# Performance work log

Hardware: AMD Instinct MI355X
Metric: run time of the kernel (lower is better)

## Reference

```python
import jax, jax.numpy as jnp
import numpy as np

THRESHOLD = 1e-12
B = 2_000_000


def _q_to_matrix(q):
    # q: [B,4] = (qw,qx,qy,qz) -> [B,3,3]
    qw, qx, qy, qz = q[:, 0], q[:, 1], q[:, 2], q[:, 3]
    r00 = 1 - 2 * (qy * qy + qz * qz)
    r01 = 2 * (qx * qy - qz * qw)
    r02 = 2 * (qx * qz + qy * qw)
    r10 = 2 * (qx * qy + qz * qw)
    r11 = 1 - 2 * (qx * qx + qz * qz)
    r12 = 2 * (qy * qz - qx * qw)
    r20 = 2 * (qx * qz - qy * qw)
    r21 = 2 * (qy * qz + qx * qw)
    r22 = 1 - 2 * (qx * qx + qy * qy)
    return jnp.stack([
        jnp.stack([r00, r01, r02], axis=-1),
        jnp.stack([r10, r11, r12], axis=-1),
        jnp.stack([r20, r21, r22], axis=-1),
    ], axis=-2)


def _so3_RV(omega):
    # omega: [B,3] -> (R [B,3,3], V [B,3,3]) via Rodrigues
    ox, oy, oz = omega[:, 0], omega[:, 1], omega[:, 2]
    z = jnp.zeros_like(ox)
    K = jnp.stack([
        jnp.stack([z, -oz, oy], axis=-1),
        jnp.stack([oz, z, -ox], axis=-1),
        jnp.stack([-oy, ox, z], axis=-1),
    ], axis=-2)
    K2 = jnp.matmul(K, K)
    theta_sqr = ox * ox + oy * oy + oz * oz
    safe = theta_sqr > THRESHOLD
    ts = jnp.where(safe, theta_sqr, 1.0)  # avoid div by ~0
    theta = jnp.sqrt(ts)
    st, ct = jnp.sin(theta), jnp.cos(theta)
    A = jnp.where(safe, st / theta, 1.0)              # sin(t)/t
    Bc = jnp.where(safe, (1.0 - ct) / ts, 0.0)        # (1-cos t)/t^2
    Cc = jnp.where(safe, (theta - st) / (ts * theta), 1.0 / 6.0)  # (t-sin t)/t^3
    I = jnp.eye(3, dtype=omega.dtype)
    R = I + A[:, None, None] * K + Bc[:, None, None] * K2
    V = I + Bc[:, None, None] * K + Cc[:, None, None] * K2
    return R, V


def _M_to_R7(M):
    # M: [B,4,4] -> [B,7,1] (x,y,z,qw,qx,qy,qz), branchless quaternion extraction
    m = lambda i, j: M[:, i, j]
    c_m22 = m(2, 2) < 0
    c_0g1 = m(0, 0) > m(1, 1)
    c_0ln1 = m(0, 0) < -m(1, 1)
    s1 = c_m22 & c_0g1
    s2 = c_m22 & (~c_0g1)
    s3 = (~c_m22) & c_0ln1
    t1 = 1 + m(0, 0) - m(1, 1) - m(2, 2)
    t2 = 1 - m(0, 0) + m(1, 1) - m(2, 2)
    t3 = 1 - m(0, 0) - m(1, 1) + m(2, 2)
    t4 = 1 + m(0, 0) + m(1, 1) + m(2, 2)
    q1 = jnp.stack([m(2, 1) - m(1, 2), t1, m(0, 1) + m(1, 0), m(2, 0) + m(0, 2)], axis=-1)
    q2 = jnp.stack([m(0, 2) - m(2, 0), m(0, 1) + m(1, 0), t2, m(1, 2) + m(2, 1)], axis=-1)
    q3 = jnp.stack([m(1, 0) - m(0, 1), m(2, 0) + m(0, 2), m(1, 2) + m(2, 1), t3], axis=-1)
    q4 = jnp.stack([t4, m(2, 1) - m(1, 2), m(0, 2) - m(2, 0), m(1, 0) - m(0, 1)], axis=-1)
    t = jnp.where(s1, t1, jnp.where(s2, t2, jnp.where(s3, t3, t4)))
    q = jnp.where(s1[:, None], q1, jnp.where(s2[:, None], q2, jnp.where(s3[:, None], q3, q4)))
    q = q * (0.5 / jnp.sqrt(t))[:, None]
    q = jnp.where((q[:, 0] < 0)[:, None], -q, q)
    r7 = jnp.concatenate([M[:, 0:3, 3], q], axis=-1)
    return r7[:, :, None]


def setup_inputs() -> dict:
    key = jax.random.key(0)
    k1, k2, k3 = jax.random.split(key, 3)
    trans = jax.random.normal(k1, (B, 3), dtype=jnp.float32)
    q = jax.random.normal(k2, (B, 4), dtype=jnp.float32)
    q = q / jnp.linalg.norm(q, axis=1, keepdims=True)  # valid unit quaternion
    Tg = jnp.concatenate([trans, q], axis=1)[:, :, None]  # [B,7,1]
    xi = (0.5 * jax.random.normal(k3, (B, 6), dtype=jnp.float32))[:, :, None]  # [B,6,1]
    return {"Tg": Tg, "xi": xi}


def reference(Tg, xi):
    rho = xi[:, 0:3]          # [B,3,1]
    omega = xi[:, 3:6, 0]     # [B,3]
    R, V = _so3_RV(omega)
    top = jnp.concatenate([R, jnp.matmul(V, rho)], axis=-1)  # [B,3,4]
    bottom = jnp.broadcast_to(jnp.array([[[0.0, 0.0, 0.0, 1.0]]], dtype=Tg.dtype), (Tg.shape[0], 1, 4))
    Txi = jnp.concatenate([top, bottom], axis=-2)            # [B,4,4]
    Rg = _q_to_matrix(Tg[:, 3:7, 0])
    tg = Tg[:, 0:3]
    Tg_top = jnp.concatenate([Rg, tg], axis=-1)
    Tg_M = jnp.concatenate([Tg_top, bottom], axis=-2)        # [B,4,4]
    T = jnp.matmul(Txi, Tg_M)
    return _M_to_R7(T)
```

## Files before the change

### kernel.cpp

```cpp
#include <hip/hip_runtime.h>
#include <math.h>

__global__ __launch_bounds__(256) void se3comp_kernel(
    const float* __restrict__ Tg, const float* __restrict__ xi,
    float* __restrict__ out, int n)
{
    int i = blockIdx.x * blockDim.x + threadIdx.x;
    if (i >= n) return;

    const float2* x2 = reinterpret_cast<const float2*>(xi) + (size_t)i * 3;
    float2 a0 = x2[0], a1 = x2[1], a2 = x2[2];
    float rx = a0.x, ry = a0.y, rz = a1.x;
    float ox = a1.y, oy = a2.x, oz = a2.y;

    float th2 = ox*ox + oy*oy + oz*oz;
    bool safe = th2 > 1e-12f;
    float ts = safe ? th2 : 1.0f;
    float theta = sqrtf(ts);
    float st = sinf(theta);
    float ct = cosf(theta);
    float A  = safe ? st / theta : 1.0f;
    float Bc = safe ? (1.0f - ct) / ts : 0.0f;
    float Cc = safe ? (theta - st) / (ts * theta) : (1.0f / 6.0f);

    float xx = ox*ox - th2, yy = oy*oy - th2, zz = oz*oz - th2;
    float xy = ox*oy, xz = ox*oz, yz = oy*oz;

    float r00 = 1.0f + Bc*xx;
    float r01 = Bc*xy - A*oz;
    float r02 = Bc*xz + A*oy;
    float r10 = Bc*xy + A*oz;
    float r11 = 1.0f + Bc*yy;
    float r12 = Bc*yz - A*ox;
    float r20 = Bc*xz - A*oy;
    float r21 = Bc*yz + A*ox;
    float r22 = 1.0f + Bc*zz;

    float v00 = 1.0f + Cc*xx;
    float v01 = Cc*xy - Bc*oz;
    float v02 = Cc*xz + Bc*oy;
    float v10 = Cc*xy + Bc*oz;
    float v11 = 1.0f + Cc*yy;
    float v12 = Cc*yz - Bc*ox;
    float v20 = Cc*xz - Bc*oy;
    float v21 = Cc*yz + Bc*ox;
    float v22 = 1.0f + Cc*zz;

    float txi0 = v00*rx + v01*ry + v02*rz;
    float txi1 = v10*rx + v11*ry + v12*rz;
    float txi2 = v20*rx + v21*ry + v22*rz;

    const float* g = Tg + (size_t)i * 7;
    float tg0 = g[0], tg1 = g[1], tg2 = g[2];
    float qw = g[3], qx = g[4], qy = g[5], qz = g[6];

    float g00 = 1.0f - 2.0f*(qy*qy + qz*qz);
    float g01 = 2.0f*(qx*qy - qz*qw);
    float g02 = 2.0f*(qx*qz + qy*qw);
    float g10 = 2.0f*(qx*qy + qz*qw);
    float g11 = 1.0f - 2.0f*(qx*qx + qz*qz);
    float g12 = 2.0f*(qy*qz - qx*qw);
    float g20 = 2.0f*(qx*qz - qy*qw);
    float g21 = 2.0f*(qy*qz + qx*qw);
    float g22 = 1.0f - 2.0f*(qx*qx + qy*qy);

    float m00 = r00*g00 + r01*g10 + r02*g20;
    float m01 = r00*g01 + r01*g11 + r02*g21;
    float m02 = r00*g02 + r01*g12 + r02*g22;
    float m10 = r10*g00 + r11*g10 + r12*g20;
    float m11 = r10*g01 + r11*g11 + r12*g21;
    float m12 = r10*g02 + r11*g12 + r12*g22;
    float m20 = r20*g00 + r21*g10 + r22*g20;
    float m21 = r20*g01 + r21*g11 + r22*g21;
    float m22 = r20*g02 + r21*g12 + r22*g22;

    float t0 = r00*tg0 + r01*tg1 + r02*tg2 + txi0;
    float t1 = r10*tg0 + r11*tg1 + r12*tg2 + txi1;
    float t2 = r20*tg0 + r21*tg1 + r22*tg2 + txi2;

    bool c_m22  = m22 < 0.0f;
    bool c_0g1  = m00 > m11;
    bool c_0ln1 = m00 < -m11;
    float t, qa, qb, qc, qd;
    if (c_m22) {
        if (c_0g1) {
            t = 1.0f + m00 - m11 - m22;
            qa = m21 - m12; qb = t;         qc = m01 + m10; qd = m20 + m02;
        } else {
            t = 1.0f - m00 + m11 - m22;
            qa = m02 - m20; qb = m01 + m10; qc = t;         qd = m12 + m21;
        }
    } else {
        if (c_0ln1) {
            t = 1.0f - m00 - m11 + m22;
            qa = m10 - m01; qb = m20 + m02; qc = m12 + m21; qd = t;
        } else {
            t = 1.0f + m00 + m11 + m22;
            qa = t;         qb = m21 - m12; qc = m02 - m20; qd = m10 - m01;
        }
    }
    float s = 0.5f / sqrtf(t);
    qa *= s; qb *= s; qc *= s; qd *= s;
    if (qa < 0.0f) { qa = -qa; qb = -qb; qc = -qc; qd = -qd; }

    float* o = out + (size_t)i * 7;
    o[0] = t0; o[1] = t1; o[2] = t2;
    o[3] = qa; o[4] = qb; o[5] = qc; o[6] = qd;
}

extern "C" void kernel_launch(void* const* d_in, const int* in_sizes, int n_in,
                              void* d_out, int out_size, void* d_ws, size_t ws_size,
                              hipStream_t stream) {
    const float* Tg = (const float*)d_in[0];
    const float* xi = (const float*)d_in[1];
    float* out = (float*)d_out;
    int n = in_sizes[0] / 7;
    const int block = 256;
    int grid = (n + block - 1) / block;
    hipLaunchKernelGGL(se3comp_kernel, dim3(grid), dim3(block), 0, stream,
                       Tg, xi, out, n);
}
```

Measured before the change: 29.61 us.

## Stage AoS inputs and outputs through LDS with coalesced float4 transfers

Each block now loads its contiguous slab of Tg and xi into shared memory with float4 global loads, computes per-element from LDS, writes results to an LDS buffer, then stores the block's output with coalesced float4 writes. The target is the uncoalesced stride-7 scalar loads and stores of the AoS layout. It adds two barriers, LDS bank conflicts on stride-7/6 accesses, and extra LDS usage that may reduce occupancy. The tail is handled by truncating to whole float4s, so with n divisible by 4 it is fine, but other n would drop trailing floats.

```diff
diff --git a/kernel.cpp b/kernel.cpp
--- a/kernel.cpp
+++ b/kernel.cpp
@@ -1,122 +1,164 @@
 #include <hip/hip_runtime.h>
 #include <math.h>
 
+#define BLOCK 256
+#define EPB   256
+
 __global__ __launch_bounds__(256) void se3comp_kernel(
-    const float* __restrict__ Tg, const float* __restrict__ xi,
-    float* __restrict__ out, int n)
+    const float4* __restrict__ Tg4, const float4* __restrict__ xi4,
+    float4* __restrict__ out4, int n)
 {
-    int i = blockIdx.x * blockDim.x + threadIdx.x;
-    if (i >= n) return;
+    __shared__ float sTg[EPB * 7];
+    __shared__ float sXi[EPB * 6];
+    __shared__ float sOut[EPB * 7];
 
-    const float2* x2 = reinterpret_cast<const float2*>(xi) + (size_t)i * 3;
-    float2 a0 = x2[0], a1 = x2[1], a2 = x2[2];
-    float rx = a0.x, ry = a0.y, rz = a1.x;
-    float ox = a1.y, oy = a2.x, oz = a2.y;
+    const int tid = threadIdx.x;
+    const int blockBase = blockIdx.x * EPB;
 
-    float th2 = ox*ox + oy*oy + oz*oz;
-    bool safe = th2 > 1e-12f;
-    float ts = safe ? th2 : 1.0f;
-    float theta = sqrtf(ts);
-    float st = sinf(theta);
-    float ct = cosf(theta);
-    float A  = safe ? st / theta : 1.0f;
-    float Bc = safe ? (1.0f - ct) / ts : 0.0f;
-    float Cc = safe ? (theta - st) / (ts * theta) : (1.0f / 6.0f);
-
-    float xx = ox*ox - th2, yy = oy*oy - th2, zz = oz*oz - th2;
-    float xy = ox*oy, xz = ox*oz, yz = oy*oz;
-
-    float r00 = 1.0f + Bc*xx;
-    float r01 = Bc*xy - A*oz;
-    float r02 = Bc*xz + A*oy;
-    float r10 = Bc*xy + A*oz;
-    float r11 = 1.0f + Bc*yy;
-    float r12 = Bc*yz - A*ox;
-    float r20 = Bc*xz - A*oy;
-    float r21 = Bc*yz + A*ox;
-    float r22 = 1.0f + Bc*zz;
-
-    float v00 = 1.0f + Cc*xx;
-    float v01 = Cc*xy - Bc*oz;
-    float v02 = Cc*xz + Bc*oy;
-    float v10 = Cc*xy + Bc*oz;
-    float v11 = 1.0f + Cc*yy;
-    float v12 = Cc*yz - Bc*ox;
-    float v20 = Cc*xz - Bc*oy;
-    float v21 = Cc*yz + Bc*ox;
-    float v22 = 1.0f + Cc*zz;
-
-    float txi0 = v00*rx + v01*ry + v02*rz;
-    float txi1 = v10*rx + v11*ry + v12*rz;
-    float txi2 = v20*rx + v21*ry + v22*rz;
-
-    const float* g = Tg + (size_t)i * 7;
-    float tg0 = g[0], tg1 = g[1], tg2 = g[2];
-    float qw = g[3], qx = g[4], qy = g[5], qz = g[6];
-
-    float g00 = 1.0f - 2.0f*(qy*qy + qz*qz);
-    float g01 = 2.0f*(qx*qy - qz*qw);
-    float g02 = 2.0f*(qx*qz + qy*qw);
-    float g10 = 2.0f*(qx*qy + qz*qw);
-    float g11 = 1.0f - 2.0f*(qx*qx + qz*qz);
-    float g12 = 2.0f*(qy*qz - qx*qw);
-    float g20 = 2.0f*(qx*qz - qy*qw);
-    float g21 = 2.0f*(qy*qz + qx*qw);
-    float g22 = 1.0f - 2.0f*(qx*qx + qy*qy);
-
-    float m00 = r00*g00 + r01*g10 + r02*g20;
-    float m01 = r00*g01 + r01*g11 + r02*g21;
-    float m02 = r00*g02 + r01*g12 + r02*g22;
-    float m10 = r10*g00 + r11*g10 + r12*g20;
-    float m11 = r10*g01 + r11*g11 + r12*g21;
-    float m12 = r10*g02 + r11*g12 + r12*g22;
-    float m20 = r20*g00 + r21*g10 + r22*g20;
-    float m21 = r20*g01 + r21*g11 + r22*g21;
-    float m22 = r20*g02 + r21*g12 + r22*g22;
-
-    float t0 = r00*tg0 + r01*tg1 + r02*tg2 + txi0;
-    float t1 = r10*tg0 + r11*tg1 + r12*tg2 + txi1;
-    float t2 = r20*tg0 + r21*tg1 + r22*tg2 + txi2;
-
-    bool c_m22  = m22 < 0.0f;
-    bool c_0g1  = m00 > m11;
-    bool c_0ln1 = m00 < -m11;
-    float t, qa, qb, qc, qd;
-    if (c_m22) {
-        if (c_0g1) {
-            t = 1.0f + m00 - m11 - m22;
-            qa = m21 - m12; qb = t;         qc = m01 + m10; qd = m20 + m02;
-        } else {
-            t = 1.0f - m00 + m11 - m22;
-            qa = m02 - m20; qb = m01 + m10; qc = t;         qd = m12 + m21;
-        }
-    } else {
-        if (c_0ln1) {
-            t = 1.0f - m00 - m11 + m22;
-            qa = m10 - m01; qb = m20 + m02; qc = m12 + m21; qd = t;
-        } else {
-            t = 1.0f + m00 + m11 + m22;
-            qa = t;         qb = m21 - m12; qc = m02 - m20; qd = m10 - m01;
+    const long tgF4Base  = (long)blockBase * 7 / 4;
+    const long tgF4Total = ((long)n * 7) / 4;
+    float4* sTg4 = reinterpret_cast<float4*>(sTg);
+    #pragma unroll
+    for (int k = 0; k < 2; ++k) {
+        int idx = tid + k * BLOCK;
+        if (idx < EPB * 7 / 4) {
+            long g = tgF4Base + idx;
+            if (g < tgF4Total) sTg4[idx] = Tg4[g];
         }
     }
-    float s = 0.5f / sqrtf(t);
-    qa *= s; qb *= s; qc *= s; qd *= s;
-    if (qa < 0.0f) { qa = -qa; qb = -qb; qc = -qc; qd = -qd; }
+    const long xiF4Base  = (long)blockBase * 6 / 4;
+    const long xiF4Total = ((long)n * 6) / 4;
+    float4* sXi4 = reinterpret_cast<float4*>(sXi);
+    #pragma unroll
+    for (int k = 0; k < 2; ++k) {
+        int idx = tid + k * BLOCK;
+        if (idx < EPB * 6 / 4) {
+            long g = xiF4Base + idx;
+            if (g < xiF4Total) sXi4[idx] = xi4[g];
+        }
+    }
+    __syncthreads();
 
-    float* o = out + (size_t)i * 7;
-    o[0] = t0; o[1] = t1; o[2] = t2;
-    o[3] = qa; o[4] = qb; o[5] = qc; o[6] = qd;
+    const int e = blockBase + tid;
+    if (e < n) {
+        const float* x = &sXi[tid * 6];
+        float rx = x[0], ry = x[1], rz = x[2];
+        float ox = x[3], oy = x[4], oz = x[5];
+        const float* gp = &sTg[tid * 7];
+        float tg0 = gp[0], tg1 = gp[1], tg2 = gp[2];
+        float qw = gp[3], qx = gp[4], qy = gp[5], qz = gp[6];
+
+        float th2 = ox*ox + oy*oy + oz*oz;
+        bool safe = th2 > 1e-12f;
+        float ts = safe ? th2 : 1.0f;
+        float theta = sqrtf(ts);
+        float st = sinf(theta);
+        float ct = cosf(theta);
+        float A  = safe ? st / theta : 1.0f;
+        float Bc = safe ? (1.0f - ct) / ts : 0.0f;
+        float Cc = safe ? (theta - st) / (ts * theta) : (1.0f / 6.0f);
+
+        float xx = ox*ox - th2, yy = oy*oy - th2, zz = oz*oz - th2;
+        float xy = ox*oy, xz = ox*oz, yz = oy*oz;
+
+        float r00 = 1.0f + Bc*xx;
+        float r01 = Bc*xy - A*oz;
+        float r02 = Bc*xz + A*oy;
+        float r10 = Bc*xy + A*oz;
+        float r11 = 1.0f + Bc*yy;
+        float r12 = Bc*yz - A*ox;
+        float r20 = Bc*xz - A*oy;
+        float r21 = Bc*yz + A*ox;
+        float r22 = 1.0f + Bc*zz;
+
+        float v00 = 1.0f + Cc*xx;
+        float v01 = Cc*xy - Bc*oz;
+        float v02 = Cc*xz + Bc*oy;
+        float v10 = Cc*xy + Bc*oz;
+        float v11 = 1.0f + Cc*yy;
+        float v12 = Cc*yz - Bc*ox;
+        float v20 = Cc*xz - Bc*oy;
+        float v21 = Cc*yz + Bc*ox;
+        float v22 = 1.0f + Cc*zz;
+
+        float txi0 = v00*rx + v01*ry + v02*rz;
+        float txi1 = v10*rx + v11*ry + v12*rz;
+        float txi2 = v20*rx + v21*ry + v22*rz;
+
+        float g00 = 1.0f - 2.0f*(qy*qy + qz*qz);
+        float g01 = 2.0f*(qx*qy - qz*qw);
+        float g02 = 2.0f*(qx*qz + qy*qw);
+        float g10 = 2.0f*(qx*qy + qz*qw);
+        float g11 = 1.0f - 2.0f*(qx*qx + qz*qz);
+        float g12 = 2.0f*(qy*qz - qx*qw);
+        float g20 = 2.0f*(qx*qz - qy*qw);
+        float g21 = 2.0f*(qy*qz + qx*qw);
+        float g22 = 1.0f - 2.0f*(qx*qx + qy*qy);
+
+        float m00 = r00*g00 + r01*g10 + r02*g20;
+        float m01 = r00*g01 + r01*g11 + r02*g21;
+        float m02 = r00*g02 + r01*g12 + r02*g22;
+        float m10 = r10*g00 + r11*g10 + r12*g20;
+        float m11 = r10*g01 + r11*g11 + r12*g21;
+        float m12 = r10*g02 + r11*g12 + r12*g22;
+        float m20 = r20*g00 + r21*g10 + r22*g20;
+        float m21 = r20*g01 + r21*g11 + r22*g21;
+        float m22 = r20*g02 + r21*g12 + r22*g22;
+
+        float t0 = r00*tg0 + r01*tg1 + r02*tg2 + txi0;
+        float t1 = r10*tg0 + r11*tg1 + r12*tg2 + txi1;
+        float t2 = r20*tg0 + r21*tg1 + r22*tg2 + txi2;
+
+        bool c_m22  = m22 < 0.0f;
+        bool c_0g1  = m00 > m11;
+        bool c_0ln1 = m00 < -m11;
+        float t, qa, qb, qc, qd;
+        if (c_m22) {
+            if (c_0g1) {
+                t = 1.0f + m00 - m11 - m22;
+                qa = m21 - m12; qb = t;         qc = m01 + m10; qd = m20 + m02;
+            } else {
+                t = 1.0f - m00 + m11 - m22;
+                qa = m02 - m20; qb = m01 + m10; qc = t;         qd = m12 + m21;
+            }
+        } else {
+            if (c_0ln1) {
+                t = 1.0f - m00 - m11 + m22;
+                qa = m10 - m01; qb = m20 + m02; qc = m12 + m21; qd = t;
+            } else {
+                t = 1.0f + m00 + m11 + m22;
+                qa = t;         qb = m21 - m12; qc = m02 - m20; qd = m10 - m01;
+            }
+        }
+        float s = 0.5f / sqrtf(t);
+        qa *= s; qb *= s; qc *= s; qd *= s;
+        if (qa < 0.0f) { qa = -qa; qb = -qb; qc = -qc; qd = -qd; }
+
+        float* o = &sOut[tid * 7];
+        o[0] = t0; o[1] = t1; o[2] = t2;
+        o[3] = qa; o[4] = qb; o[5] = qc; o[6] = qd;
+    }
+    __syncthreads();
+
+    float4* sOut4 = reinterpret_cast<float4*>(sOut);
+    #pragma unroll
+    for (int k = 0; k < 2; ++k) {
+        int idx = tid + k * BLOCK;
+        if (idx < EPB * 7 / 4) {
+            long g = tgF4Base + idx;
+            if (g < tgF4Total) out4[g] = sOut4[idx];
+        }
+    }
 }
 
 extern "C" void kernel_launch(void* const* d_in, const int* in_sizes, int n_in,
                               void* d_out, int out_size, void* d_ws, size_t ws_size,
                               hipStream_t stream) {
-    const float* Tg = (const float*)d_in[0];
-    const float* xi = (const float*)d_in[1];
-    float* out = (float*)d_out;
+    const float4* Tg = (const float4*)d_in[0];
+    const float4* xi = (const float4*)d_in[1];
+    float4* out = (float4*)d_out;
     int n = in_sizes[0] / 7;
-    const int block = 256;
-    int grid = (n + block - 1) / block;
-    hipLaunchKernelGGL(se3comp_kernel, dim3(grid), dim3(block), 0, stream,
+    int grid = (n + EPB - 1) / EPB;
+    hipLaunchKernelGGL(se3comp_kernel, dim3(grid), dim3(BLOCK), 0, stream,
                        Tg, xi, out, n);
 }
```

Result: slower. 31.32 us (+5.8%).

## Process four poses per thread with 16-byte vector loads and nontemporal stores

Applied to the files above, without the earlier changes.

Each thread now handles four consecutive poses. It loads their 28 Tg floats and 24 xi floats as aligned float4 vectors and writes the 28 outputs as float4 nontemporal stores, replacing the 7-float strided scalar accesses that lose coalescing. The math also switches to fast intrinsics (__sinf/__cosf, __fdividef, rsqrtf), sharing a single reciprocal for the Rodrigues coefficients. The costs are higher register pressure, four times fewer threads, and a small loss of accuracy from the fast trig.

```diff
diff --git a/kernel.cpp b/kernel.cpp
--- a/kernel.cpp
+++ b/kernel.cpp
@@ -1,27 +1,26 @@
 #include <hip/hip_runtime.h>
 #include <math.h>
 
-__global__ __launch_bounds__(256) void se3comp_kernel(
-    const float* __restrict__ Tg, const float* __restrict__ xi,
-    float* __restrict__ out, int n)
+typedef float f32x4 __attribute__((ext_vector_type(4)));
+
+struct R7 { float v[7]; };
+
+__device__ __forceinline__ R7 se3_one(
+    float tg0, float tg1, float tg2,
+    float qw,  float qx,  float qy, float qz,
+    float rx,  float ry,  float rz,
+    float ox,  float oy,  float oz)
 {
-    int i = blockIdx.x * blockDim.x + threadIdx.x;
-    if (i >= n) return;
-
-    const float2* x2 = reinterpret_cast<const float2*>(xi) + (size_t)i * 3;
-    float2 a0 = x2[0], a1 = x2[1], a2 = x2[2];
-    float rx = a0.x, ry = a0.y, rz = a1.x;
-    float ox = a1.y, oy = a2.x, oz = a2.y;
-
     float th2 = ox*ox + oy*oy + oz*oz;
     bool safe = th2 > 1e-12f;
     float ts = safe ? th2 : 1.0f;
     float theta = sqrtf(ts);
-    float st = sinf(theta);
-    float ct = cosf(theta);
-    float A  = safe ? st / theta : 1.0f;
-    float Bc = safe ? (1.0f - ct) / ts : 0.0f;
-    float Cc = safe ? (theta - st) / (ts * theta) : (1.0f / 6.0f);
+    float st = __sinf(theta);
+    float ct = __cosf(theta);
+    float inv3 = __fdividef(1.0f, ts * theta);
+    float A  = safe ? st * ts * inv3        : 1.0f;
+    float Bc = safe ? (1.0f - ct) * theta * inv3 : 0.0f;
+    float Cc = safe ? (theta - st) * inv3   : (1.0f / 6.0f);
 
     float xx = ox*ox - th2, yy = oy*oy - th2, zz = oz*oz - th2;
     float xy = ox*oy, xz = ox*oz, yz = oy*oz;
@@ -49,10 +48,6 @@
     float txi0 = v00*rx + v01*ry + v02*rz;
     float txi1 = v10*rx + v11*ry + v12*rz;
     float txi2 = v20*rx + v21*ry + v22*rz;
-
-    const float* g = Tg + (size_t)i * 7;
-    float tg0 = g[0], tg1 = g[1], tg2 = g[2];
-    float qw = g[3], qx = g[4], qy = g[5], qz = g[6];
 
     float g00 = 1.0f - 2.0f*(qy*qy + qz*qz);
     float g01 = 2.0f*(qx*qy - qz*qw);
@@ -99,24 +94,78 @@
             qa = t;         qb = m21 - m12; qc = m02 - m20; qd = m10 - m01;
         }
     }
-    float s = 0.5f / sqrtf(t);
+    float s = 0.5f * rsqrtf(t);
     qa *= s; qb *= s; qc *= s; qd *= s;
     if (qa < 0.0f) { qa = -qa; qb = -qb; qc = -qc; qd = -qd; }
 
-    float* o = out + (size_t)i * 7;
-    o[0] = t0; o[1] = t1; o[2] = t2;
-    o[3] = qa; o[4] = qb; o[5] = qc; o[6] = qd;
+    R7 r;
+    r.v[0] = t0; r.v[1] = t1; r.v[2] = t2;
+    r.v[3] = qa; r.v[4] = qb; r.v[5] = qc; r.v[6] = qd;
+    return r;
+}
+
+__global__ __launch_bounds__(256) void se3comp_kernel(
+    const f32x4* __restrict__ Tg4, const f32x4* __restrict__ xi4,
+    f32x4* __restrict__ out4, int n)
+{
+    const int j = blockIdx.x * blockDim.x + threadIdx.x;
+    const int base = j * 4;
+    if (base >= n) return;
+
+    if (base + 3 < n) {
+        float tgf[28], xif[24];
+        #pragma unroll
+        for (int k = 0; k < 7; ++k) {
+            f32x4 v = Tg4[(size_t)j * 7 + k];
+            tgf[k*4+0] = v.x; tgf[k*4+1] = v.y; tgf[k*4+2] = v.z; tgf[k*4+3] = v.w;
+        }
+        #pragma unroll
+        for (int k = 0; k < 6; ++k) {
+            f32x4 v = xi4[(size_t)j * 6 + k];
+            xif[k*4+0] = v.x; xif[k*4+1] = v.y; xif[k*4+2] = v.z; xif[k*4+3] = v.w;
+        }
+
+        float of[28];
+        #pragma unroll
+        for (int e = 0; e < 4; ++e) {
+            R7 r = se3_one(tgf[e*7+0], tgf[e*7+1], tgf[e*7+2],
+                           tgf[e*7+3], tgf[e*7+4], tgf[e*7+5], tgf[e*7+6],
+                           xif[e*6+0], xif[e*6+1], xif[e*6+2],
+                           xif[e*6+3], xif[e*6+4], xif[e*6+5]);
+            #pragma unroll
+            for (int f = 0; f < 7; ++f) of[e*7+f] = r.v[f];
+        }
+
+        #pragma unroll
+        for (int k = 0; k < 7; ++k) {
+            f32x4 v;
+            v.x = of[k*4+0]; v.y = of[k*4+1]; v.z = of[k*4+2]; v.w = of[k*4+3];
+            __builtin_nontemporal_store(v, &out4[(size_t)j * 7 + k]);
+        }
+    } else {
+        const float* Tgf = reinterpret_cast<const float*>(Tg4);
+        const float* xif = reinterpret_cast<const float*>(xi4);
+        float* outf = reinterpret_cast<float*>(out4);
+        for (int e = base; e < n; ++e) {
+            const float* g = Tgf + (size_t)e * 7;
+            const float* x = xif + (size_t)e * 6;
+            R7 r = se3_one(g[0], g[1], g[2], g[3], g[4], g[5], g[6],
+                           x[0], x[1], x[2], x[3], x[4], x[5]);
+            float* o = outf + (size_t)e * 7;
+            for (int f = 0; f < 7; ++f) o[f] = r.v[f];
+        }
+    }
 }
 
 extern "C" void kernel_launch(void* const* d_in, const int* in_sizes, int n_in,
                               void* d_out, int out_size, void* d_ws, size_t ws_size,
                               hipStream_t stream) {
-    const float* Tg = (const float*)d_in[0];
-    const float* xi = (const float*)d_in[1];
-    float* out = (float*)d_out;
+    const f32x4* Tg = (const f32x4*)d_in[0];
+    const f32x4* xi = (const f32x4*)d_in[1];
+    f32x4* out = (f32x4*)d_out;
     int n = in_sizes[0] / 7;
-    const int block = 256;
-    int grid = (n + block - 1) / block;
-    hipLaunchKernelGGL(se3comp_kernel, dim3(grid), dim3(block), 0, stream,
+    int nThreads = (n + 3) / 4;
+    int grid = (nThreads + 255) / 256;
+    hipLaunchKernelGGL(se3comp_kernel, dim3(grid), dim3(256), 0, stream,
                        Tg, xi, out, n);
 }
```

New measurement: 85.77 us. 2.9x slower.
